# Performance work log

Measured on AMD Instinct MI355X. Metric: run time of the kernel, lower is better.

The kernel has to match this reference:

```python
import jax, jax.numpy as jnp
import numpy as np

B, S, D = 4, 1024, 64
NEG = -1e9


def setup_inputs() -> dict:
    key = jax.random.key(0)
    ks = jax.random.split(key, 5)
    x = jax.random.normal(ks[0], (B, S, D), dtype=jnp.float32)
    # nn.Linear weights are [out_features, in_features]
    Wq = jax.random.normal(ks[1], (D, D), dtype=jnp.float32) / np.sqrt(D)
    Wk = jax.random.normal(ks[2], (D, D), dtype=jnp.float32) / np.sqrt(D)
    bk = jax.random.normal(ks[3], (D,), dtype=jnp.float32) / np.sqrt(D)
    Wv = jax.random.normal(ks[4], (D, D), dtype=jnp.float32) / np.sqrt(D)
    attn_w = jnp.ones((3,), dtype=jnp.float32)
    attn_scale = jnp.ones((1,), dtype=jnp.float32)
    return {"x": x, "Wq": Wq, "Wk": Wk, "bk": bk, "Wv": Wv,
            "attn_w": attn_w, "attn_scale": attn_scale}


def reference(x, Wq, Wk, bk, Wv, attn_w, attn_scale):
    b, s, d = x.shape
    tril = jnp.tril(jnp.ones((s, s), dtype=bool))  # causal mask, shared by all branches

    # --- branch 1: plain causal self-attention on raw x ---
    s1 = jnp.einsum('bqd,bkd->bqk', x, x)
    s1 = jnp.where(tril, s1, NEG)
    o1 = jnp.einsum('bqk,bkd->bqd', jax.nn.softmax(s1, axis=-1), x)

    # --- branch 2: scaled dot-product attention with learned extra scale ---
    q = x @ Wq.T
    k = x @ Wk.T + bk
    v = x @ Wv.T
    inv_sqrt_d = 1.0 / float(np.sqrt(d))
    s2 = jnp.einsum('bqd,bkd->bqk', q, k) * inv_sqrt_d * attn_scale[0]
    s2 = jnp.where(tril, s2, NEG)
    o2 = jnp.einsum('bqk,bkd->bqd', jax.nn.softmax(s2, axis=-1), v)

    # --- branch 3: additive (Bahdanau-style) attention ---
    # materializes [B,S,S,D] via broadcast, as in the original
    s3 = jnp.sum(jnp.tanh(x[:, :, None, :] + x[:, None, :, :]), axis=-1)
    s3 = jnp.where(tril, s3, NEG)
    o3 = jnp.einsum('bqk,bkd->bqd', jax.nn.softmax(s3, axis=-1), x)

    w = attn_w / attn_w.sum()
    return o1 * w[0] + o2 * w[1] + o3 * w[2]


if __name__ == "__main__":
    out = reference(**setup_inputs())
    print(out.shape, out.dtype)
```

## Files before the change

### kernel.cpp

```cpp
#include <hip/hip_runtime.h>
#include <hip/hip_bf16.h>

#define BB 4
#define SS 1024
#define NSD (BB*SS*64)

typedef __attribute__((ext_vector_type(4))) float f32x4;
typedef __attribute__((ext_vector_type(8))) short bf16x8;

__device__ __forceinline__ float fast_exp2(float x) { return __builtin_amdgcn_exp2f(x); }
__device__ __forceinline__ float fast_rcp(float x)  { return __builtin_amdgcn_rcpf(x); }

__device__ __forceinline__ unsigned short f2bf(float f) {
    unsigned int u = __builtin_bit_cast(unsigned int, f);
    u += 0x7fffu + ((u >> 16) & 1u);
    return (unsigned short)(u >> 16);
}
__device__ __forceinline__ float bf2f(unsigned short u) {
    unsigned int v = (unsigned int)u << 16;
    return __builtin_bit_cast(float, v);
}

__device__ __forceinline__ float sig4(const f32x4 eq, const f32x4 ek) {
    float A = __builtin_fmaf(eq[0], ek[0], 1.0f);
    float B = __builtin_fmaf(eq[1], ek[1], 1.0f);
    float C = __builtin_fmaf(eq[2], ek[2], 1.0f);
    float D = __builtin_fmaf(eq[3], ek[3], 1.0f);
    float AB = A*B, CD = C*D;
    float num = __builtin_fmaf(A+B, CD, (C+D)*AB);
    return num * fast_rcp(AB*CD);
}

__global__ __launch_bounds__(256) void k_proj(
    const float* __restrict__ x, const float* __restrict__ Wq,
    const float* __restrict__ Wk, const float* __restrict__ bkv,
    const float* __restrict__ Wv,
    unsigned short* __restrict__ qh, unsigned short* __restrict__ ql,
    unsigned short* __restrict__ kh, unsigned short* __restrict__ kl,
    unsigned short* __restrict__ xh, unsigned short* __restrict__ xlo,
    float* __restrict__ exf,
    unsigned short* __restrict__ xT, unsigned short* __restrict__ vT)
{
    __shared__ float xsh[4*68];
    const int t = threadIdx.x;
    const int r = t & 3, cc = t >> 2;
    const int row0 = blockIdx.x * 4;
    if (t < 64) {
        const int rr = t >> 4, seg = (t & 15) * 4;
        *(f32x4*)(xsh + rr*68 + seg) =
            *(const f32x4*)(x + (size_t)(row0 + rr)*64 + seg);
    }
    __syncthreads();

    const float* wqp = Wq + cc*64;
    const float* wkp = Wk + cc*64;
    const float* wvp = Wv + cc*64;
    float aq = 0.f, ak = 0.f, av = 0.f;
    #pragma unroll 4
    for (int e0 = 0; e0 < 64; e0 += 4) {
        f32x4 xv = *(const f32x4*)(xsh + r*68 + e0);
        f32x4 q4 = *(const f32x4*)(wqp + e0);
        f32x4 k4 = *(const f32x4*)(wkp + e0);
        f32x4 v4 = *(const f32x4*)(wvp + e0);
        #pragma unroll
        for (int u = 0; u < 4; ++u) {
            aq = __builtin_fmaf(xv[u], q4[u], aq);
            ak = __builtin_fmaf(xv[u], k4[u], ak);
            av = __builtin_fmaf(xv[u], v4[u], av);
        }
    }
    const int row = row0 + r;
    const int b = row >> 10, srow = row & 1023;
    const float C2 = 2.8853900817779268f;
    ak += bkv[cc];
    const size_t idx = (size_t)row*64 + cc;
    unsigned short h;
    h = f2bf(aq); qh[idx] = h; ql[idx] = f2bf(aq - bf2f(h));
    h = f2bf(ak); kh[idx] = h; kl[idx] = f2bf(ak - bf2f(h));
    const float xv_ = xsh[r*68 + cc];
    h = f2bf(xv_); xh[idx] = h; xlo[idx] = f2bf(xv_ - bf2f(h));
    exf[idx] = fast_exp2(C2 * xv_);
    xT[((size_t)b*64 + cc)*1024 + srow] = h;
    vT[((size_t)b*64 + cc)*1024 + srow] = f2bf(av);
}

__global__ __launch_bounds__(256) void k_fused(
    const unsigned short* __restrict__ xh, const unsigned short* __restrict__ xlo,
    const unsigned short* __restrict__ qh, const unsigned short* __restrict__ ql,
    const unsigned short* __restrict__ kh, const unsigned short* __restrict__ kl,
    const float* __restrict__ exf,
    const unsigned short* __restrict__ xT, const unsigned short* __restrict__ vT,
    const float* __restrict__ attn_scale,
    float* __restrict__ po, float* __restrict__ lb)
{
    __shared__ float smem[12928];
    const int t = threadIdx.x;
    const int bx = blockIdx.x;
    const int lane = t & 63, wv = t >> 6;
    const int l15 = lane & 15, g = lane >> 4;
    const float LOG2E = 1.4426950408889634f;

    if (bx < 576) {
        const int b = bx / 144;
        int rr = bx % 144;
        int qt32 = 31;
        while (rr >= ((qt32 >> 2) + 1)) { rr -= (qt32 >> 2) + 1; --qt32; }
        const int cg = rr;
        const int q0 = qt32 * 32;
        const int c = cg*4 + wv;
        const bool active = (c <= qt32);
        const int kc = c * 32;
        const int l7 = lane & 7, lk3 = lane >> 3;

        float* eqs = smem;
        float* ekw = smem + 2048 + wv*2048;
        unsigned short* Plw = (unsigned short*)(smem + 2048 + 8192) + wv*1280;
        float* lpart = smem + 2048 + 8192 + 2560;

        {
            const float* src = exf + ((size_t)b*SS + q0)*64;
            #pragma unroll
            for (int ii = 0; ii < 2; ++ii) {
                const int idx = t + 256*ii;
                const int r0 = idx >> 4, mq = idx & 15;
                *(f32x4*)(eqs + r0*64 + ((mq ^ (r0 & 7)) << 2)) =
                    *(const f32x4*)(src + r0*64 + mq*4);
            }
        }
        if (active) {
            const float* srck = exf + ((size_t)b*SS + kc)*64;
            #pragma unroll
            for (int ii = 0; ii < 8; ++ii) {
                const int idx = lane + 64*ii;
                const int r0 = idx >> 4, mq = idx & 15;
                *(f32x4*)(ekw + r0*64 + ((mq ^ (r0 & 7)) << 2)) =
                    *(const f32x4*)(srck + r0*64 + mq*4);
            }
        }
        __syncthreads();

        f32x4 acc[2][4];
        #pragma unroll
        for (int a_ = 0; a_ < 2; ++a_)
            #pragma unroll
            for (int d_ = 0; d_ < 4; ++d_)
                acc[a_][d_] = (f32x4){0.f,0.f,0.f,0.f};
        float lrow[4] = {0.f,0.f,0.f,0.f};

        if (active) {
            float ar[4][4] = {};
            #pragma unroll 4
            for (int m = 0; m < 16; ++m) {
                const int oq = (m ^ l7) << 2;
                const int ok = (m ^ lk3) << 2;
                f32x4 eqv[4], ekv[4];
                #pragma unroll
                for (int i = 0; i < 4; ++i)
                    eqv[i] = *(const f32x4*)(eqs + (l7 + 8*i)*64 + oq);
                #pragma unroll
                for (int j = 0; j < 4; ++j)
                    ekv[j] = *(const f32x4*)(ekw + (lk3 + 8*j)*64 + ok);
                #pragma unroll
                for (int i = 0; i < 4; ++i)
                    #pragma unroll
                    for (int j = 0; j < 4; ++j)
                        ar[i][j] += sig4(eqv[i], ekv[j]);
            }
            #pragma unroll
            for (int i = 0; i < 4; ++i) {
                const int q = q0 + l7 + 8*i;
                #pragma unroll
                for (int j = 0; j < 4; ++j) {
                    const int k = kc + lk3 + 8*j;
                    float e = (k <= q)
                        ? fast_exp2(__builtin_fmaf(ar[i][j], -2.8853900817779268f,
                                                   46.166241308446475f))
                        : 0.f;
                    lrow[i] += e;
                    Plw[(l7 + 8*i)*40 + lk3 + 8*j] = f2bf(e);
                }
            }
            const unsigned short* vb = xT + (size_t)b*64*1024;
            #pragma unroll
            for (int qh2 = 0; qh2 < 2; ++qh2) {
                bf16x8 af = *(const bf16x8*)(Plw + (qh2*16 + l15)*40 + g*8);
                #pragma unroll
                for (int db = 0; db < 4; ++db) {
                    bf16x8 bf_ = *(const bf16x8*)(vb + (size_t)(db*16 + l15)*1024 + kc + g*8);
                    acc[qh2][db] = __builtin_amdgcn_mfma_f32_16x16x32_bf16(af, bf_, acc[qh2][db], 0, 0, 0);
                }
            }
        }
        #pragma unroll
        for (int i = 0; i < 4; ++i) {
            lrow[i] += __shfl_xor(lrow[i], 8, 64);
            lrow[i] += __shfl_xor(lrow[i], 16, 64);
            lrow[i] += __shfl_xor(lrow[i], 32, 64);
        }
        if (lane < 8) {
            #pragma unroll
            for (int i = 0; i < 4; ++i) lpart[wv*32 + l7 + 8*i] = lrow[i];
        }
        #pragma unroll
        for (int qh2 = 0; qh2 < 2; ++qh2)
            #pragma unroll
            for (int db = 0; db < 4; ++db)
                #pragma unroll
                for (int i = 0; i < 4; ++i) {
                    const int row = qh2*16 + g*4 + i;
                    const int col = db*16 + l15;
                    const int L = (row << 4) + (col >> 2);
                    const int P = L ^ ((L >> 3) & 7);
                    ekw[(P << 2) + (col & 3)] = acc[qh2][db][i];
                }
        __syncthreads();
        {
            const int L0 = t*2,     P0 = L0 ^ ((L0 >> 3) & 7);
            const int L1 = t*2 + 1, P1 = L1 ^ ((L1 >> 3) & 7);
            f32x4 s0 = {0,0,0,0}, s1 = {0,0,0,0};
            #pragma unroll
            for (int w = 0; w < 4; ++w) {
                const float* ob = smem + 2048 + w*2048;
                s0 += *(const f32x4*)(ob + (P0 << 2));
                s1 += *(const f32x4*)(ob + (P1 << 2));
            }
            float* pob = po + (size_t)(4+cg)*NSD + ((size_t)b*SS + q0)*64;
            *(f32x4*)(pob + (size_t)(L0 >> 4)*64 + (L0 & 15)*4) = s0;
            *(f32x4*)(pob + (size_t)(L1 >> 4)*64 + (L1 & 15)*4) = s1;
            if (t < 32) {
                float l = lpart[t] + lpart[32 + t] + lpart[64 + t] + lpart[96 + t];
                lb[(size_t)(4+cg)*(BB*SS) + (size_t)b*SS + q0 + t] = l;
            }
        }
    } else {
        unsigned short* Pl = (unsigned short*)smem;
        float* lpart = smem + 1024;
        const int y = bx - 576;
        const int split = y & 1, b = (y >> 1) & 3;
        const int qt = 63 - ((y >> 3) & 63);
        const int br = (y >> 9) & 1;
        const int q0 = qt * 16;
        const int nc = (qt >> 2) + 1;

        const unsigned short* Ah_p = (br ? qh : xh) + ((size_t)b*SS + q0)*64;
        const unsigned short* Al_p = (br ? ql : xlo) + ((size_t)b*SS + q0)*64;
        const unsigned short* Bh_p = (br ? kh : xh) + (size_t)b*SS*64;
        const unsigned short* Bl_p = (br ? kl : xlo) + (size_t)b*SS*64;
        const unsigned short* Vb   = (br ? vT : xT) + (size_t)b*64*1024;

        const int ko = g * 8;
        bf16x8 Ah0 = *(const bf16x8*)(Ah_p + (size_t)l15*64 + ko);
        bf16x8 Ah1 = *(const bf16x8*)(Ah_p + (size_t)l15*64 + 32 + ko);
        bf16x8 Al0 = *(const bf16x8*)(Al_p + (size_t)l15*64 + ko);
        bf16x8 Al1 = *(const bf16x8*)(Al_p + (size_t)l15*64 + 32 + ko);

        const float pscale = br ? (0.125f * attn_scale[0] * LOG2E) : LOG2E;
        const float pshift = br ? 0.f : (-64.f * LOG2E);

        f32x4 lacc = {0,0,0,0};
        f32x4 oacc = {0,0,0,0};

        for (int cc2 = split; cc2 < nc; cc2 += 2) {
            const int kc = cc2 * 64;
            const int krow = kc + wv*16 + l15;
            bf16x8 Bh0 = *(const bf16x8*)(Bh_p + (size_t)krow*64 + ko);
            bf16x8 Bh1 = *(const bf16x8*)(Bh_p + (size_t)krow*64 + 32 + ko);
            bf16x8 Bl0 = *(const bf16x8*)(Bl_p + (size_t)krow*64 + ko);
            bf16x8 Bl1 = *(const bf16x8*)(Bl_p + (size_t)krow*64 + 32 + ko);
            f32x4 s = {0,0,0,0};
            s = __builtin_amdgcn_mfma_f32_16x16x32_bf16(Ah0, Bh0, s, 0, 0, 0);
            s = __builtin_amdgcn_mfma_f32_16x16x32_bf16(Ah1, Bh1, s, 0, 0, 0);
            s = __builtin_amdgcn_mfma_f32_16x16x32_bf16(Ah0, Bl0, s, 0, 0, 0);
            s = __builtin_amdgcn_mfma_f32_16x16x32_bf16(Ah1, Bl1, s, 0, 0, 0);
            s = __builtin_amdgcn_mfma_f32_16x16x32_bf16(Al0, Bh0, s, 0, 0, 0);
            s = __builtin_amdgcn_mfma_f32_16x16x32_bf16(Al1, Bh1, s, 0, 0, 0);
            const int kg = kc + wv*16 + l15;
            #pragma unroll
            for (int i = 0; i < 4; ++i) {
                const int q = q0 + g*4 + i;
                float e = (kg <= q) ? fast_exp2(__builtin_fmaf(s[i], pscale, pshift)) : 0.f;
                lacc[i] += e;
                Pl[(g*4+i)*72 + wv*16 + l15] = f2bf(e);
            }
            __syncthreads();
            #pragma unroll
            for (int ks = 0; ks < 2; ++ks) {
                bf16x8 af = *(const bf16x8*)(Pl + l15*72 + ks*32 + g*8);
                bf16x8 bf_ = *(const bf16x8*)(Vb + (size_t)(wv*16 + l15)*1024 + kc + ks*32 + g*8);
                oacc = __builtin_amdgcn_mfma_f32_16x16x32_bf16(af, bf_, oacc, 0, 0, 0);
            }
            __syncthreads();
        }
        #pragma unroll
        for (int off = 8; off >= 1; off >>= 1) {
            lacc[0] += __shfl_xor(lacc[0], off, 64);
            lacc[1] += __shfl_xor(lacc[1], off, 64);
            lacc[2] += __shfl_xor(lacc[2], off, 64);
            lacc[3] += __shfl_xor(lacc[3], off, 64);
        }
        if (l15 == 0) {
            #pragma unroll
            for (int i = 0; i < 4; ++i) lpart[wv*16 + g*4 + i] = lacc[i];
        }
        __syncthreads();
        const size_t slot = (size_t)(br*2 + split);
        if (t < 16) {
            float l = lpart[t] + lpart[16 + t] + lpart[32 + t] + lpart[48 + t];
            lb[slot*((size_t)BB*SS) + (size_t)b*SS + q0 + t] = l;
        }
        float* pob = po + slot*((size_t)NSD) + ((size_t)b*SS + q0)*64;
        #pragma unroll
        for (int i = 0; i < 4; ++i)
            pob[(size_t)(g*4 + i)*64 + wv*16 + l15] = oacc[i];
    }
}

__global__ __launch_bounds__(256) void k_comb(
    const float* __restrict__ po, const float* __restrict__ lb,
    const float* __restrict__ attn_w, float* __restrict__ out)
{
    const int v = blockIdx.x*256 + threadIdx.x;
    const int qg = v >> 4;
    const int ns = ((qg & 1023) >> 7) + 1;
    const float aw0 = attn_w[0], aw1 = attn_w[1], aw2 = attn_w[2];
    const float iws = fast_rcp(aw0 + aw1 + aw2);
    const f32x4* p = (const f32x4*)po;
    const int NQ = BB*SS;

    f32x4 s01 = p[(size_t)0*65536 + v] + p[(size_t)1*65536 + v];
    f32x4 s23 = p[(size_t)2*65536 + v] + p[(size_t)3*65536 + v];
    f32x4 s3s = {0,0,0,0};
    float l3 = 0.f;
    #pragma unroll
    for (int s = 0; s < 8; ++s) {
        if (s < ns) {
            s3s += p[(size_t)(4+s)*65536 + v];
            l3 += lb[(4+s)*NQ + qg];
        }
    }
    const float f0 = aw0 * iws * fast_rcp(lb[0*NQ + qg] + lb[1*NQ + qg]);
    const float f1 = aw1 * iws * fast_rcp(lb[2*NQ + qg] + lb[3*NQ + qg]);
    const float f2 = aw2 * iws * fast_rcp(l3);
    f32x4 o;
    #pragma unroll
    for (int u = 0; u < 4; ++u)
        o[u] = __builtin_fmaf(s01[u], f0,
               __builtin_fmaf(s23[u], f1, s3s[u]*f2));
    ((f32x4*)out)[v] = o;
}

extern "C" void kernel_launch(void* const* d_in, const int* in_sizes, int n_in,
                              void* d_out, int out_size, void* d_ws, size_t ws_size,
                              hipStream_t stream) {
    (void)in_sizes; (void)n_in; (void)out_size; (void)ws_size;
    const float* x          = (const float*)d_in[0];
    const float* Wq         = (const float*)d_in[1];
    const float* Wk         = (const float*)d_in[2];
    const float* bk         = (const float*)d_in[3];
    const float* Wv         = (const float*)d_in[4];
    const float* attn_w     = (const float*)d_in[5];
    const float* attn_scale = (const float*)d_in[6];
    float* out              = (float*)d_out;

    float* exf = (float*)d_ws;
    unsigned short* qh  = (unsigned short*)(exf + NSD);
    unsigned short* ql  = qh  + NSD;
    unsigned short* kh  = ql  + NSD;
    unsigned short* kl  = kh  + NSD;
    unsigned short* xh  = kl  + NSD;
    unsigned short* xlo = xh  + NSD;
    unsigned short* xT  = xlo + NSD;
    unsigned short* vT  = xT  + NSD;
    float* po = (float*)(vT + NSD);
    float* lb = po + (size_t)12*NSD;

    k_proj <<<1024, 256, 0, stream>>>(x, Wq, Wk, bk, Wv,
                                      qh, ql, kh, kl, xh, xlo, exf, xT, vT);
    k_fused<<<1600, 256, 0, stream>>>(xh, xlo, qh, ql, kh, kl, exf, xT, vT,
                                      attn_scale, po, lb);
    k_comb <<<256, 256, 0, stream>>>(po, lb, attn_w, out);
}
```

Measured before the change: 52.07 us.

## Store exp table in bf16, drop in-block wave reduction, write per-wave partials

The exp(2x) table is now stored and staged in bf16 instead of fp32, which halves global and LDS traffic for the additive-attention branch and unpacks pairs in registers. Each wave now writes its own partial output and row sum directly to a separate slot (32 slots instead of 8). This removes the LDS cross-wave reduction and the second barrier. The combine kernel loops over a variable number of slots per query band. In exchange the partial buffer grows several-fold, combine reads more data, and bf16 rounding of exp(2x) reduces precision of the tanh scores.

```diff
diff --git a/kernel.cpp b/kernel.cpp
--- a/kernel.cpp
+++ b/kernel.cpp
@@ -6,6 +6,7 @@
 #define NSD (BB*SS*64)
 
 typedef __attribute__((ext_vector_type(4))) float f32x4;
+typedef __attribute__((ext_vector_type(4))) unsigned int u32x4;
 typedef __attribute__((ext_vector_type(8))) short bf16x8;
 
 __device__ __forceinline__ float fast_exp2(float x) { return __builtin_amdgcn_exp2f(x); }
@@ -31,6 +32,15 @@
     return num * fast_rcp(AB*CD);
 }
 
+__device__ __forceinline__ void unpack8(bf16x8 v, f32x4& e, f32x4& o) {
+    u32x4 u = __builtin_bit_cast(u32x4, v);
+    #pragma unroll
+    for (int i = 0; i < 4; ++i) {
+        e[i] = __builtin_bit_cast(float, u[i] << 16);
+        o[i] = __builtin_bit_cast(float, u[i] & 0xFFFF0000u);
+    }
+}
+
 __global__ __launch_bounds__(256) void k_proj(
     const float* __restrict__ x, const float* __restrict__ Wq,
     const float* __restrict__ Wk, const float* __restrict__ bkv,
@@ -38,7 +48,7 @@
     unsigned short* __restrict__ qh, unsigned short* __restrict__ ql,
     unsigned short* __restrict__ kh, unsigned short* __restrict__ kl,
     unsigned short* __restrict__ xh, unsigned short* __restrict__ xlo,
-    float* __restrict__ exf,
+    unsigned short* __restrict__ exfb,
     unsigned short* __restrict__ xT, unsigned short* __restrict__ vT)
 {
     __shared__ float xsh[4*68];
@@ -79,7 +89,7 @@
     h = f2bf(ak); kh[idx] = h; kl[idx] = f2bf(ak - bf2f(h));
     const float xv_ = xsh[r*68 + cc];
     h = f2bf(xv_); xh[idx] = h; xlo[idx] = f2bf(xv_ - bf2f(h));
-    exf[idx] = fast_exp2(C2 * xv_);
+    exfb[idx] = f2bf(fast_exp2(C2 * xv_));
     xT[((size_t)b*64 + cc)*1024 + srow] = h;
     vT[((size_t)b*64 + cc)*1024 + srow] = f2bf(av);
 }
@@ -88,12 +98,12 @@
     const unsigned short* __restrict__ xh, const unsigned short* __restrict__ xlo,
     const unsigned short* __restrict__ qh, const unsigned short* __restrict__ ql,
     const unsigned short* __restrict__ kh, const unsigned short* __restrict__ kl,
-    const float* __restrict__ exf,
+    const unsigned short* __restrict__ exfb,
     const unsigned short* __restrict__ xT, const unsigned short* __restrict__ vT,
     const float* __restrict__ attn_scale,
     float* __restrict__ po, float* __restrict__ lb)
 {
-    __shared__ float smem[12928];
+    __shared__ __align__(16) unsigned short smem[15360];
     const int t = threadIdx.x;
     const int bx = blockIdx.x;
     const int lane = t & 63, wv = t >> 6;
@@ -112,60 +122,50 @@
         const int kc = c * 32;
         const int l7 = lane & 7, lk3 = lane >> 3;
 
-        float* eqs = smem;
-        float* ekw = smem + 2048 + wv*2048;
-        unsigned short* Plw = (unsigned short*)(smem + 2048 + 8192) + wv*1280;
-        float* lpart = smem + 2048 + 8192 + 2560;
+        unsigned short* eqb = smem;
+        unsigned short* ekw = smem + 2048 + wv*2048;
+        unsigned short* Plw = smem + 10240 + wv*1280;
 
         {
-            const float* src = exf + ((size_t)b*SS + q0)*64;
-            #pragma unroll
-            for (int ii = 0; ii < 2; ++ii) {
-                const int idx = t + 256*ii;
-                const int r0 = idx >> 4, mq = idx & 15;
-                *(f32x4*)(eqs + r0*64 + ((mq ^ (r0 & 7)) << 2)) =
-                    *(const f32x4*)(src + r0*64 + mq*4);
-            }
+            const int r0 = t >> 3, o0 = t & 7;
+            *(bf16x8*)(eqb + r0*64 + ((o0 ^ (r0 & 7)) << 3)) =
+                *(const bf16x8*)(exfb + ((size_t)b*SS + q0 + r0)*64 + o0*8);
         }
         if (active) {
-            const float* srck = exf + ((size_t)b*SS + kc)*64;
-            #pragma unroll
-            for (int ii = 0; ii < 8; ++ii) {
-                const int idx = lane + 64*ii;
-                const int r0 = idx >> 4, mq = idx & 15;
-                *(f32x4*)(ekw + r0*64 + ((mq ^ (r0 & 7)) << 2)) =
-                    *(const f32x4*)(srck + r0*64 + mq*4);
+            #pragma unroll
+            for (int ii = 0; ii < 4; ++ii) {
+                const int jdx = lane + 64*ii;
+                const int r0 = jdx >> 3, o0 = jdx & 7;
+                *(bf16x8*)(ekw + r0*64 + ((o0 ^ (r0 & 7)) << 3)) =
+                    *(const bf16x8*)(exfb + ((size_t)b*SS + kc + r0)*64 + o0*8);
             }
         }
         __syncthreads();
-
-        f32x4 acc[2][4];
-        #pragma unroll
-        for (int a_ = 0; a_ < 2; ++a_)
-            #pragma unroll
-            for (int d_ = 0; d_ < 4; ++d_)
-                acc[a_][d_] = (f32x4){0.f,0.f,0.f,0.f};
-        float lrow[4] = {0.f,0.f,0.f,0.f};
 
         if (active) {
             float ar[4][4] = {};
-            #pragma unroll 4
-            for (int m = 0; m < 16; ++m) {
-                const int oq = (m ^ l7) << 2;
-                const int ok = (m ^ lk3) << 2;
-                f32x4 eqv[4], ekv[4];
-                #pragma unroll
-                for (int i = 0; i < 4; ++i)
-                    eqv[i] = *(const f32x4*)(eqs + (l7 + 8*i)*64 + oq);
-                #pragma unroll
-                for (int j = 0; j < 4; ++j)
-                    ekv[j] = *(const f32x4*)(ekw + (lk3 + 8*j)*64 + ok);
+            #pragma unroll
+            for (int m8 = 0; m8 < 8; ++m8) {
+                const int oq = (m8 ^ l7) << 3;
+                const int ok = (m8 ^ lk3) << 3;
+                f32x4 eqe[4], eqo[4], eke[4], eko[4];
+                #pragma unroll
+                for (int i = 0; i < 4; ++i) {
+                    bf16x8 v = *(const bf16x8*)(eqb + (l7 + 8*i)*64 + oq);
+                    unpack8(v, eqe[i], eqo[i]);
+                }
+                #pragma unroll
+                for (int j = 0; j < 4; ++j) {
+                    bf16x8 v = *(const bf16x8*)(ekw + (lk3 + 8*j)*64 + ok);
+                    unpack8(v, eke[j], eko[j]);
+                }
                 #pragma unroll
                 for (int i = 0; i < 4; ++i)
                     #pragma unroll
                     for (int j = 0; j < 4; ++j)
-                        ar[i][j] += sig4(eqv[i], ekv[j]);
-            }
+                        ar[i][j] += sig4(eqe[i], eke[j]) + sig4(eqo[i], eko[j]);
+            }
+            float lrow[4] = {0.f,0.f,0.f,0.f};
             #pragma unroll
             for (int i = 0; i < 4; ++i) {
                 const int q = q0 + l7 + 8*i;
@@ -180,6 +180,18 @@
                     Plw[(l7 + 8*i)*40 + lk3 + 8*j] = f2bf(e);
                 }
             }
+            #pragma unroll
+            for (int i = 0; i < 4; ++i) {
+                lrow[i] += __shfl_xor(lrow[i], 8, 64);
+                lrow[i] += __shfl_xor(lrow[i], 16, 64);
+                lrow[i] += __shfl_xor(lrow[i], 32, 64);
+            }
+            f32x4 acc[2][4];
+            #pragma unroll
+            for (int a_ = 0; a_ < 2; ++a_)
+                #pragma unroll
+                for (int d_ = 0; d_ < 4; ++d_)
+                    acc[a_][d_] = (f32x4){0.f,0.f,0.f,0.f};
             const unsigned short* vb = xT + (size_t)b*64*1024;
             #pragma unroll
             for (int qh2 = 0; qh2 < 2; ++qh2) {
@@ -190,51 +202,26 @@
                     acc[qh2][db] = __builtin_amdgcn_mfma_f32_16x16x32_bf16(af, bf_, acc[qh2][db], 0, 0, 0);
                 }
             }
-        }
-        #pragma unroll
-        for (int i = 0; i < 4; ++i) {
-            lrow[i] += __shfl_xor(lrow[i], 8, 64);
-            lrow[i] += __shfl_xor(lrow[i], 16, 64);
-            lrow[i] += __shfl_xor(lrow[i], 32, 64);
-        }
-        if (lane < 8) {
-            #pragma unroll
-            for (int i = 0; i < 4; ++i) lpart[wv*32 + l7 + 8*i] = lrow[i];
-        }
-        #pragma unroll
-        for (int qh2 = 0; qh2 < 2; ++qh2)
-            #pragma unroll
-            for (int db = 0; db < 4; ++db)
+            const size_t slot = 4 + c;
+            if (lane < 8) {
+                #pragma unroll
+                for (int i = 0; i < 4; ++i)
+                    lb[slot*(size_t)(BB*SS) + (size_t)b*SS + q0 + l7 + 8*i] = lrow[i];
+            }
+            float* pob = po + slot*(size_t)NSD + ((size_t)b*SS + q0)*64;
+            #pragma unroll
+            for (int qh2 = 0; qh2 < 2; ++qh2)
                 #pragma unroll
                 for (int i = 0; i < 4; ++i) {
                     const int row = qh2*16 + g*4 + i;
-                    const int col = db*16 + l15;
-                    const int L = (row << 4) + (col >> 2);
-                    const int P = L ^ ((L >> 3) & 7);
-                    ekw[(P << 2) + (col & 3)] = acc[qh2][db][i];
-                }
-        __syncthreads();
-        {
-            const int L0 = t*2,     P0 = L0 ^ ((L0 >> 3) & 7);
-            const int L1 = t*2 + 1, P1 = L1 ^ ((L1 >> 3) & 7);
-            f32x4 s0 = {0,0,0,0}, s1 = {0,0,0,0};
-            #pragma unroll
-            for (int w = 0; w < 4; ++w) {
-                const float* ob = smem + 2048 + w*2048;
-                s0 += *(const f32x4*)(ob + (P0 << 2));
-                s1 += *(const f32x4*)(ob + (P1 << 2));
-            }
-            float* pob = po + (size_t)(4+cg)*NSD + ((size_t)b*SS + q0)*64;
-            *(f32x4*)(pob + (size_t)(L0 >> 4)*64 + (L0 & 15)*4) = s0;
-            *(f32x4*)(pob + (size_t)(L1 >> 4)*64 + (L1 & 15)*4) = s1;
-            if (t < 32) {
-                float l = lpart[t] + lpart[32 + t] + lpart[64 + t] + lpart[96 + t];
-                lb[(size_t)(4+cg)*(BB*SS) + (size_t)b*SS + q0 + t] = l;
-            }
+                    #pragma unroll
+                    for (int db = 0; db < 4; ++db)
+                        pob[(size_t)row*64 + db*16 + l15] = acc[qh2][db][i];
+                }
         }
     } else {
-        unsigned short* Pl = (unsigned short*)smem;
-        float* lpart = smem + 1024;
+        unsigned short* Pl = smem;
+        float* lpart = (float*)(smem + 2048);
         const int y = bx - 576;
         const int split = y & 1, b = (y >> 1) & 3;
         const int qt = 63 - ((y >> 3) & 63);
@@ -321,7 +308,7 @@
 {
     const int v = blockIdx.x*256 + threadIdx.x;
     const int qg = v >> 4;
-    const int ns = ((qg & 1023) >> 7) + 1;
+    const int band = (qg & 1023) >> 5;
     const float aw0 = attn_w[0], aw1 = attn_w[1], aw2 = attn_w[2];
     const float iws = fast_rcp(aw0 + aw1 + aw2);
     const f32x4* p = (const f32x4*)po;
@@ -331,12 +318,9 @@
     f32x4 s23 = p[(size_t)2*65536 + v] + p[(size_t)3*65536 + v];
     f32x4 s3s = {0,0,0,0};
     float l3 = 0.f;
-    #pragma unroll
-    for (int s = 0; s < 8; ++s) {
-        if (s < ns) {
-            s3s += p[(size_t)(4+s)*65536 + v];
-            l3 += lb[(4+s)*NQ + qg];
-        }
+    for (int s = 0; s <= band; ++s) {
+        s3s += p[(size_t)(4+s)*65536 + v];
+        l3 += lb[(4+s)*NQ + qg];
     }
     const float f0 = aw0 * iws * fast_rcp(lb[0*NQ + qg] + lb[1*NQ + qg]);
     const float f1 = aw1 * iws * fast_rcp(lb[2*NQ + qg] + lb[3*NQ + qg]);
@@ -362,8 +346,8 @@
     const float* attn_scale = (const float*)d_in[6];
     float* out              = (float*)d_out;
 
-    float* exf = (float*)d_ws;
-    unsigned short* qh  = (unsigned short*)(exf + NSD);
+    unsigned short* exfb = (unsigned short*)d_ws;
+    unsigned short* qh  = exfb + NSD;
     unsigned short* ql  = qh  + NSD;
     unsigned short* kh  = ql  + NSD;
     unsigned short* kl  = kh  + NSD;
@@ -372,11 +356,11 @@
     unsigned short* xT  = xlo + NSD;
     unsigned short* vT  = xT  + NSD;
     float* po = (float*)(vT + NSD);
-    float* lb = po + (size_t)12*NSD;
+    float* lb = po + (size_t)36*NSD;
 
     k_proj <<<1024, 256, 0, stream>>>(x, Wq, Wk, bk, Wv,
-                                      qh, ql, kh, kl, xh, xlo, exf, xT, vT);
-    k_fused<<<1600, 256, 0, stream>>>(xh, xlo, qh, ql, kh, kl, exf, xT, vT,
+                                      qh, ql, kh, kl, xh, xlo, exfb, xT, vT);
+    k_fused<<<1600, 256, 0, stream>>>(xh, xlo, qh, ql, kh, kl, exfb, xT, vT,
                                       attn_scale, po, lb);
     k_comb <<<256, 256, 0, stream>>>(po, lb, attn_w, out);
 }
```

Result: slower. 76.31 us (+46.6%).
